# Kernel optimization log

Measured on AMD Instinct MI355X. Metric: run time of the kernel, lower is better.

## Reference

```python
import jax, jax.numpy as jnp
import numpy as np

EPS = 1e-5

def rotate_half(x):
    # interleaved pairs: (..., d*2) -> stack(-x2, x1) interleaved back
    x = x.reshape(*x.shape[:-1], -1, 2)
    x1, x2 = x[..., 0], x[..., 1]
    return jnp.stack((-x2, x1), axis=-1).reshape(*x.shape[:-2], -1)

def apply_rotary(freqs, x):
    # freqs: (b, n, d); x: (b, h, n, d) -> broadcast over heads (unsqueeze at dim=1)
    f = freqs[:, None, :, :]
    return x * jnp.cos(f) + rotate_half(x) * jnp.sin(f)

def layer_norm(x, g, b):
    mu = jnp.mean(x, axis=-1, keepdims=True)
    var = jnp.var(x, axis=-1, keepdims=True)
    return (x - mu) * jax.lax.rsqrt(var + EPS) * g + b

def setup_inputs() -> dict:
    key = jax.random.key(0)
    ks = jax.random.split(key, 10)
    b, nq, nkv, dim, h, dh = 8, 1024, 2048, 512, 8, 64
    inner = h * dh
    return {
        "x_query": jax.random.normal(ks[0], (b, nq, dim), jnp.float32),
        "x_context": jax.random.normal(ks[1], (b, nkv, dim), jnp.float32),
        "rotary_time_emb_query": jax.random.normal(ks[2], (b, nq, dh), jnp.float32),
        "rotary_time_emb_context": jax.random.normal(ks[3], (b, nkv, dh), jnp.float32),
        "context_mask": jnp.ones((b, nkv), dtype=bool),
        "ln_q_g": jnp.ones((dim,), jnp.float32),
        "ln_q_b": jnp.zeros((dim,), jnp.float32),
        "ln_c_g": jnp.ones((dim,), jnp.float32),
        "ln_c_b": jnp.zeros((dim,), jnp.float32),
        "Wq": jax.random.normal(ks[4], (dim, inner), jnp.float32) * 0.02,
        "Wkv": jax.random.normal(ks[5], (dim, 2 * inner), jnp.float32) * 0.02,
        "Wo": jax.random.normal(ks[6], (inner, dim), jnp.float32) * 0.02,
        "bo": jnp.zeros((dim,), jnp.float32),
    }

def reference(x_query, x_context, rotary_time_emb_query, rotary_time_emb_context,
              context_mask, ln_q_g, ln_q_b, ln_c_g, ln_c_b, Wq, Wkv, Wo, bo):
    h = 8
    xq = layer_norm(x_query, ln_q_g, ln_q_b)
    xc = layer_norm(x_context, ln_c_g, ln_c_b)
    q = xq @ Wq                       # (b, nq, inner)
    kv = xc @ Wkv                     # (b, nkv, 2*inner)
    k, v = jnp.split(kv, 2, axis=-1)
    split_heads = lambda t: t.reshape(t.shape[0], t.shape[1], h, -1).transpose(0, 2, 1, 3)
    q, k, v = split_heads(q), split_heads(k), split_heads(v)  # (b, h, n, dh)
    q = apply_rotary(rotary_time_emb_query, q)
    k = apply_rotary(rotary_time_emb_context, k)
    v = apply_rotary(rotary_time_emb_context, v)   # rotate_value=True
    dh = q.shape[-1]
    scale = 1.0 / jnp.sqrt(jnp.float32(dh))
    scores = jnp.einsum('bhqd,bhkd->bhqk', q, k) * scale
    neg = jnp.finfo(scores.dtype).min
    scores = jnp.where(context_mask[:, None, None, :], scores, neg)
    attn = jax.nn.softmax(scores, axis=-1)
    out = jnp.einsum('bhqk,bhkd->bhqd', attn, v)
    out = apply_rotary(-rotary_time_emb_query, out)  # inverse rotation
    out = out.transpose(0, 2, 1, 3).reshape(out.shape[0], out.shape[2], -1)  # (b, nq, inner)
    return out @ Wo + bo
```

## Files before the change

### kernel.cpp

```cpp
#include <hip/hip_runtime.h>
#include <hip/hip_bf16.h>
#include <math.h>

#define BB 8
#define NQ 1024
#define NKV 2048
#define DIM 512
#define H 8
#define DH 64
#define INNER 512
#define SCALE_LOG2E 0.18033688011112042f

typedef __bf16 bf16x8 __attribute__((ext_vector_type(8)));
typedef float f32x4 __attribute__((ext_vector_type(4)));
typedef unsigned int u32x4 __attribute__((ext_vector_type(4)));

__device__ __forceinline__ unsigned short f2bf(float f) {
  union { float f; unsigned int u; } v; v.f = f;
  unsigned int r = v.u + 0x7fffu + ((v.u >> 16) & 1u);
  return (unsigned short)(r >> 16);
}
__device__ __forceinline__ float bf2f(unsigned short h) {
  union { unsigned int u; float f; } v; v.u = ((unsigned int)h) << 16;
  return v.f;
}

__global__ __launch_bounds__(256) void prep_weights(
    const float* __restrict__ Wq, const float* __restrict__ Wkv,
    const float* __restrict__ Wo,
    unsigned short* __restrict__ WqT, unsigned short* __restrict__ WkvT,
    unsigned short* __restrict__ WohT, unsigned short* __restrict__ WolT) {
  __shared__ float T[64][65];
  int blk = blockIdx.x;
  const float* src; int Wd, ti, tj, mode;
  unsigned short* dst = nullptr;
  if (blk < 64) { src = Wq;  dst = WqT;  Wd = 512;  ti = blk >> 3; tj = blk & 7; mode = 0; }
  else if (blk < 192) { int b2 = blk - 64; src = Wkv; dst = WkvT; Wd = 1024; ti = b2 >> 4; tj = b2 & 15; mode = 0; }
  else { int b2 = blk - 192; src = Wo; Wd = 512; ti = b2 >> 3; tj = b2 & 7; mode = 1; }
  int t = threadIdx.x;
#pragma unroll
  for (int i = 0; i < 16; ++i) {
    int idx = i * 256 + t;
    int r = idx >> 6, c = idx & 63;
    T[r][c] = src[(size_t)(ti * 64 + r) * Wd + tj * 64 + c];
  }
  __syncthreads();
#pragma unroll
  for (int i = 0; i < 16; ++i) {
    int idx = i * 256 + t;
    int n = idx >> 6, k = idx & 63;
    float v = T[k][n];
    size_t off = (size_t)(tj * 64 + n) * 512 + ti * 64 + k;
    if (mode == 0) {
      dst[off] = f2bf(v);
    } else {
      unsigned short hb = f2bf(v);
      WohT[off] = hb;
      WolT[off] = f2bf(v - bf2f(hb));
    }
  }
}

__global__ __launch_bounds__(256) void ln_kernel(
    const float* __restrict__ xq, const float* __restrict__ xc,
    const float* __restrict__ gq, const float* __restrict__ bq,
    const float* __restrict__ gc, const float* __restrict__ bc,
    unsigned short* __restrict__ xq_bf, unsigned short* __restrict__ xc_bf) {
  int row = blockIdx.x;
  const float* x; const float* g; const float* bb; unsigned short* out;
  if (row < BB * NQ) {
    x = xq + (size_t)row * DIM; g = gq; bb = bq; out = xq_bf + (size_t)row * DIM;
  } else {
    int r = row - BB * NQ;
    x = xc + (size_t)r * DIM; g = gc; bb = bc; out = xc_bf + (size_t)r * DIM;
  }
  int t = threadIdx.x;
  float2 v = *reinterpret_cast<const float2*>(x + t * 2);
  float s = v.x + v.y;
  float ss = v.x * v.x + v.y * v.y;
#pragma unroll
  for (int d = 1; d < 64; d <<= 1) { s += __shfl_xor(s, d); ss += __shfl_xor(ss, d); }
  __shared__ float red[8];
  int wid = t >> 6, lane = t & 63;
  if (lane == 0) { red[wid] = s; red[4 + wid] = ss; }
  __syncthreads();
  s = red[0] + red[1] + red[2] + red[3];
  ss = red[4] + red[5] + red[6] + red[7];
  float mu = s * (1.0f / DIM);
  float var = ss * (1.0f / DIM) - mu * mu;
  float rs = rsqrtf(var + 1e-5f);
  float y0 = (v.x - mu) * rs * g[t * 2] + bb[t * 2];
  float y1 = (v.y - mu) * rs * g[t * 2 + 1] + bb[t * 2 + 1];
  ushort2 o; o.x = f2bf(y0); o.y = f2bf(y1);
  *reinterpret_cast<ushort2*>(out + t * 2) = o;
}

__device__ __forceinline__ void gemm_mainloop(
    const unsigned short* __restrict__ A, const unsigned short* __restrict__ WT,
    unsigned short* As, unsigned short* Ws, float (*Cs)[66],
    int rowBase, int colBase) {
  const int t = threadIdx.x;
  const int w = t >> 6;
  const int l = t & 63;
  const int l15 = l & 15;
  const int lg = l >> 4;
  const int c7 = l15 & 7;
  f32x4 acc[4];
#pragma unroll
  for (int ct = 0; ct < 4; ++ct) acc[ct] = f32x4{0.f, 0.f, 0.f, 0.f};
  const int arow = t >> 2;
  const int aseg = (t & 3) * 16;
  const int sdst0 = arow * 64 + ((2 * (t & 3)) ^ (arow & 7)) * 8;
  const int afrag = (lg ^ c7) * 8;
  const int ard = (w * 16 + l15) * 64 + afrag;
  const unsigned short* gab = A + (size_t)(rowBase + arow) * 512 + aseg;
  const unsigned short* gwb = WT + (size_t)(colBase + arow) * 512 + aseg;
  bf16x8 ar0 = *reinterpret_cast<const bf16x8*>(gab);
  bf16x8 ar1 = *reinterpret_cast<const bf16x8*>(gab + 8);
  bf16x8 wr0 = *reinterpret_cast<const bf16x8*>(gwb);
  bf16x8 wr1 = *reinterpret_cast<const bf16x8*>(gwb + 8);
  for (int kb = 0; kb < 512; kb += 64) {
    *reinterpret_cast<bf16x8*>(&As[sdst0])     = ar0;
    *reinterpret_cast<bf16x8*>(&As[sdst0 ^ 8]) = ar1;
    *reinterpret_cast<bf16x8*>(&Ws[sdst0])     = wr0;
    *reinterpret_cast<bf16x8*>(&Ws[sdst0 ^ 8]) = wr1;
    __syncthreads();
    if (kb + 64 < 512) {
      ar0 = *reinterpret_cast<const bf16x8*>(gab + kb + 64);
      ar1 = *reinterpret_cast<const bf16x8*>(gab + kb + 72);
      wr0 = *reinterpret_cast<const bf16x8*>(gwb + kb + 64);
      wr1 = *reinterpret_cast<const bf16x8*>(gwb + kb + 72);
    }
#pragma unroll
    for (int ks = 0; ks < 2; ++ks) {
      bf16x8 af = *reinterpret_cast<const bf16x8*>(&As[ard ^ (ks ? 32 : 0)]);
#pragma unroll
      for (int ct = 0; ct < 4; ++ct) {
        bf16x8 bfr = *reinterpret_cast<const bf16x8*>(
            &Ws[(ct * 16 + l15) * 64 + (afrag ^ (ks ? 32 : 0))]);
        acc[ct] = __builtin_amdgcn_mfma_f32_16x16x32_bf16(af, bfr, acc[ct], 0, 0, 0);
      }
    }
    __syncthreads();
  }
#pragma unroll
  for (int ct = 0; ct < 4; ++ct)
#pragma unroll
    for (int r = 0; r < 4; ++r)
      Cs[w * 16 + lg * 4 + r][ct * 16 + l15] = acc[ct][r];
  __syncthreads();
}

__global__ __launch_bounds__(256) void proj_q(
    const unsigned short* __restrict__ xq_bf, const unsigned short* __restrict__ WqT,
    const float* __restrict__ rotq, unsigned short* __restrict__ Qb) {
  __shared__ unsigned short As[64 * 64];
  __shared__ unsigned short Ws[64 * 64];
  __shared__ float Cs[64][66];
  int o = blockIdx.x;
  int swz = ((o & 7) << 7) + (o >> 3);
  int bn = swz & 7, bm = swz >> 3;
  gemm_mainloop(xq_bf, WqT, As, Ws, Cs, bm * 64, bn * 64);
  int t = threadIdx.x;
#pragma unroll
  for (int i = 0; i < 8; ++i) {
    int p = i * 256 + t;
    int row = p >> 5, pc = p & 31, d0 = pc * 2;
    int grow = bm * 64 + row;
    float c0 = Cs[row][d0], c1 = Cs[row][d0 + 1];
    const float* f = rotq + (size_t)grow * DH + d0;
    float f0 = f[0], f1 = f[1], s0, s1, co0, co1;
    __sincosf(f0, &s0, &co0);
    __sincosf(f1, &s1, &co1);
    float o0 = (c0 * co0 - c1 * s0) * SCALE_LOG2E;
    float o1 = (c1 * co1 + c0 * s1) * SCALE_LOG2E;
    ushort2 ov; ov.x = f2bf(o0); ov.y = f2bf(o1);
    int b = grow >> 10, qq = grow & 1023;
    *reinterpret_cast<ushort2*>(Qb + (((size_t)(b * H + bn) * NQ + qq) * DH + d0)) = ov;
  }
}

__global__ __launch_bounds__(256) void proj_kv(
    const unsigned short* __restrict__ xc_bf, const unsigned short* __restrict__ WkvT,
    const float* __restrict__ rotc, unsigned short* __restrict__ Kb,
    unsigned short* __restrict__ VTb) {
  __shared__ unsigned short As[64 * 64];
  __shared__ unsigned short Ws[64 * 64];
  __shared__ float Cs[64][66];
  int o = blockIdx.x;
  int swz = ((o & 7) << 9) + (o >> 3);
  int bn = swz & 15, bm = swz >> 4;
  gemm_mainloop(xc_bf, WkvT, As, Ws, Cs, bm * 64, bn * 64);
  int t = threadIdx.x;
  int h = bn & 7;
  int b = bm >> 5, chunk = bm & 31;
  if (bn < 8) {
#pragma unroll
    for (int i = 0; i < 8; ++i) {
      int p = i * 256 + t;
      int row = p >> 5, pc = p & 31, d0 = pc * 2;
      int grow = bm * 64 + row;
      float c0 = Cs[row][d0], c1 = Cs[row][d0 + 1];
      const float* f = rotc + (size_t)grow * DH + d0;
      float f0 = f[0], f1 = f[1], s0, s1, co0, co1;
      __sincosf(f0, &s0, &co0);
      __sincosf(f1, &s1, &co1);
      float o0 = c0 * co0 - c1 * s0;
      float o1 = c1 * co1 + c0 * s1;
      int kk = grow & 2047;
      ushort2 ov; ov.x = f2bf(o0); ov.y = f2bf(o1);
      *reinterpret_cast<ushort2*>(Kb + (((size_t)(b * H + h) * NKV + kk) * DH + d0)) = ov;
    }
  } else {
    unsigned short* vbase = VTb + (((size_t)(b * H + h) * 32 + chunk) * 64) * 64;
    int oc = t & 7;
    int dd0 = t >> 3;
#pragma unroll
    for (int half = 0; half < 2; ++half) {
      int d = dd0 + half * 32;
      u32x4 pack;
#pragma unroll
      for (int j2 = 0; j2 < 4; ++j2) {
        unsigned int lohi[2];
#pragma unroll
        for (int e = 0; e < 2; ++e) {
          int p = oc * 8 + j2 * 2 + e;
          int pp = p & 31;
          int kv = (p >> 5) * 32 + ((pp & 1) ? ((pp >> 1) + 16) : (pp >> 1));
          float c0 = Cs[kv][d], cx = Cs[kv][d ^ 1];
          float f = rotc[(size_t)(bm * 64 + kv) * DH + d];
          float sn, cs;
          __sincosf(f, &sn, &cs);
          float val = (d & 1) ? (c0 * cs + cx * sn) : (c0 * cs - cx * sn);
          lohi[e] = f2bf(val);
        }
        pack[j2] = lohi[0] | (lohi[1] << 16);
      }
      *reinterpret_cast<u32x4*>(vbase + d * 64 + oc * 8) = pack;
    }
  }
}

__global__ __launch_bounds__(256) void attn_kernel(
    const unsigned short* __restrict__ Qb, const unsigned short* __restrict__ Kb,
    const unsigned short* __restrict__ VTb, const int* __restrict__ mask,
    const float* __restrict__ rotq,
    unsigned short* __restrict__ Ahb, unsigned short* __restrict__ Alb) {
  __shared__ unsigned short Ks[64 * 64];
  __shared__ unsigned short Vs[64 * 64];
  __shared__ unsigned short Ps[4 * 16 * 64];
  __shared__ float Ms[NKV];
  int ob = blockIdx.x;
  int swz = ((ob & 7) << 7) + (ob >> 3);
  int qb = swz & 15;
  int bh = swz >> 4;
  int b = bh >> 3, hh = bh & 7;
  int t = threadIdx.x, w = t >> 6, l = t & 63;
  int l15 = l & 15, lg = l >> 4;
  int c7 = l15 & 7;

  {
    const int* mrow = mask + b * NKV;
    int4 m0 = *reinterpret_cast<const int4*>(mrow + t * 8);
    int4 m1 = *reinterpret_cast<const int4*>(mrow + t * 8 + 4);
    Ms[t * 8 + 0] = m0.x ? 1.f : 0.f;
    Ms[t * 8 + 1] = m0.y ? 1.f : 0.f;
    Ms[t * 8 + 2] = m0.z ? 1.f : 0.f;
    Ms[t * 8 + 3] = m0.w ? 1.f : 0.f;
    Ms[t * 8 + 4] = m1.x ? 1.f : 0.f;
    Ms[t * 8 + 5] = m1.y ? 1.f : 0.f;
    Ms[t * 8 + 6] = m1.z ? 1.f : 0.f;
    Ms[t * 8 + 7] = m1.w ? 1.f : 0.f;
  }

  const unsigned short* qrow = Qb + ((size_t)bh * NQ + qb * 64 + w * 16 + l15) * DH;
  bf16x8 qa0 = *reinterpret_cast<const bf16x8*>(qrow + lg * 8);
  bf16x8 qa1 = *reinterpret_cast<const bf16x8*>(qrow + 32 + lg * 8);

  float plsum[4] = {0.f, 0.f, 0.f, 0.f};
  f32x4 acc[4];
#pragma unroll
  for (int ct = 0; ct < 4; ++ct) acc[ct] = f32x4{0.f, 0.f, 0.f, 0.f};

  const int srow = t >> 2;
  const int sseg = (t & 3) * 16;
  const int sdst0 = srow * 64 + ((2 * (t & 3)) ^ (srow & 7)) * 8;
  const int frag = (lg ^ c7) * 8;
  const int kbase = l15 * 64 + frag;
  const int prbase = w * 1024 + l15 * 64 + frag;
  unsigned int* pw = reinterpret_cast<unsigned int*>(Ps);
  const int lg4 = lg * 4, l3 = l15 & 3, sD = l15 >> 2;

  const unsigned short* gk = Kb + ((size_t)bh * NKV + srow) * DH + sseg;
  const unsigned short* gv = VTb + (((size_t)bh * 32) * 64 + srow) * 64 + sseg;

  bf16x8 kr0 = *reinterpret_cast<const bf16x8*>(gk);
  bf16x8 kr1 = *reinterpret_cast<const bf16x8*>(gk + 8);
  bf16x8 vr0 = *reinterpret_cast<const bf16x8*>(gv);
  bf16x8 vr1 = *reinterpret_cast<const bf16x8*>(gv + 8);
  gk += 4096; gv += 4096;

  for (int ic = 0; ic < NKV / 64; ++ic) {
    *reinterpret_cast<bf16x8*>(&Ks[sdst0])     = kr0;
    *reinterpret_cast<bf16x8*>(&Ks[sdst0 ^ 8]) = kr1;
    *reinterpret_cast<bf16x8*>(&Vs[sdst0])     = vr0;
    *reinterpret_cast<bf16x8*>(&Vs[sdst0 ^ 8]) = vr1;
    __syncthreads();
    if (ic + 1 < NKV / 64) {
      kr0 = *reinterpret_cast<const bf16x8*>(gk);
      kr1 = *reinterpret_cast<const bf16x8*>(gk + 8);
      vr0 = *reinterpret_cast<const bf16x8*>(gv);
      vr1 = *reinterpret_cast<const bf16x8*>(gv + 8);
      gk += 4096; gv += 4096;
    }
    f32x4 s[4];
    __builtin_amdgcn_s_setprio(1);
#pragma unroll
    for (int tt = 0; tt < 4; ++tt) {
      f32x4 z = f32x4{0.f, 0.f, 0.f, 0.f};
      bf16x8 k0 = *reinterpret_cast<const bf16x8*>(&Ks[tt * 1024 + kbase]);
      z = __builtin_amdgcn_mfma_f32_16x16x32_bf16(qa0, k0, z, 0, 0, 0);
      bf16x8 k1 = *reinterpret_cast<const bf16x8*>(&Ks[tt * 1024 + (kbase ^ 32)]);
      z = __builtin_amdgcn_mfma_f32_16x16x32_bf16(qa1, k1, z, 0, 0, 0);
      s[tt] = z;
    }
    __builtin_amdgcn_s_setprio(0);
    float mv[4];
#pragma unroll
    for (int tt = 0; tt < 4; ++tt) mv[tt] = Ms[ic * 64 + tt * 16 + l15];
    float p[4][4];
#pragma unroll
    for (int tt = 0; tt < 4; ++tt)
#pragma unroll
      for (int r = 0; r < 4; ++r) {
        float e;
        asm("v_exp_f32 %0, %1" : "=v"(e) : "v"(s[tt][r]));
        p[tt][r] = e * mv[tt];
      }
#pragma unroll
    for (int r = 0; r < 4; ++r)
      plsum[r] += (p[0][r] + p[1][r]) + (p[2][r] + p[3][r]);
#pragma unroll
    for (int r = 0; r < 4; ++r) {
      unsigned int d01, d23;
      asm("v_cvt_pk_bf16_f32 %0, %1, %2" : "=v"(d01) : "v"(p[0][r]), "v"(p[1][r]));
      asm("v_cvt_pk_bf16_f32 %0, %1, %2" : "=v"(d23) : "v"(p[2][r]), "v"(p[3][r]));
      int row = lg4 + r;
      int rb = row & 7;
      int dwl = ((sD ^ rb) << 2) + l3;
      int pb = w * 512 + row * 32 + dwl;
      pw[pb] = d01;
      pw[pb ^ 16] = d23;
    }
    asm volatile("s_waitcnt lgkmcnt(0)" ::: "memory");
    __builtin_amdgcn_sched_barrier(0);
    __builtin_amdgcn_s_setprio(1);
#pragma unroll
    for (int ks = 0; ks < 2; ++ks) {
      bf16x8 pa = *reinterpret_cast<const bf16x8*>(&Ps[(prbase ^ (ks ? 32 : 0))]);
#pragma unroll
      for (int ct = 0; ct < 4; ++ct) {
        bf16x8 vb = *reinterpret_cast<const bf16x8*>(
            &Vs[ct * 1024 + (kbase ^ (ks ? 32 : 0))]);
        acc[ct] = __builtin_amdgcn_mfma_f32_16x16x32_bf16(pa, vb, acc[ct], 0, 0, 0);
      }
    }
    __builtin_amdgcn_s_setprio(0);
    __syncthreads();
  }
#pragma unroll
  for (int d = 1; d < 16; d <<= 1)
#pragma unroll
    for (int r = 0; r < 4; ++r) plsum[r] += __shfl_xor(plsum[r], d);
  float inv[4];
#pragma unroll
  for (int r = 0; r < 4; ++r) inv[r] = 1.0f / plsum[r];

  int q0 = qb * 64 + w * 16 + lg * 4;
#pragma unroll
  for (int r = 0; r < 4; ++r) {
    int grow = b * NQ + q0 + r;
    const float* frow = rotq + (size_t)grow * DH;
    size_t obase = (size_t)grow * INNER + hh * DH;
#pragma unroll
    for (int ct = 0; ct < 4; ++ct) {
      int d = ct * 16 + l15;
      float x = acc[ct][r] * inv[r];
      float nb = __shfl_xor(x, 1);
      float f = frow[d];
      float sn, cs;
      __sincosf(f, &sn, &cs);
      float ov = (d & 1) ? (x * cs - nb * sn) : (x * cs + nb * sn);
      unsigned short hb = f2bf(ov);
      Ahb[obase + d] = hb;
      Alb[obase + d] = f2bf(ov - bf2f(hb));
    }
  }
}

__global__ __launch_bounds__(256) void final_gemm(
    const unsigned short* __restrict__ Ah, const unsigned short* __restrict__ Al,
    const unsigned short* __restrict__ Wh, const unsigned short* __restrict__ Wl,
    const float* __restrict__ bo, float* __restrict__ out) {
  __shared__ unsigned short AhS[64 * 64];
  __shared__ unsigned short AlS[64 * 64];
  __shared__ unsigned short WhS[64 * 64];
  __shared__ unsigned short WlS[64 * 64];
  int o = blockIdx.x;
  int swz = ((o & 7) << 7) + (o >> 3);
  int bn = swz & 7, bm = swz >> 3;
  const int t = threadIdx.x;
  const int w = t >> 6, l = t & 63;
  const int l15 = l & 15, lg = l >> 4, c7 = l15 & 7;
  f32x4 acc[4];
#pragma unroll
  for (int ct = 0; ct < 4; ++ct) acc[ct] = f32x4{0.f, 0.f, 0.f, 0.f};
  const int arow = t >> 2;
  const int aseg = (t & 3) * 16;
  const int sdst0 = arow * 64 + ((2 * (t & 3)) ^ (arow & 7)) * 8;
  const int afrag = (lg ^ c7) * 8;
  const int ard = (w * 16 + l15) * 64 + afrag;
  const unsigned short* gah = Ah + (size_t)(bm * 64 + arow) * 512 + aseg;
  const unsigned short* gal = Al + (size_t)(bm * 64 + arow) * 512 + aseg;
  const unsigned short* gwh = Wh + (size_t)(bn * 64 + arow) * 512 + aseg;
  const unsigned short* gwl = Wl + (size_t)(bn * 64 + arow) * 512 + aseg;
  bf16x8 rah0 = *reinterpret_cast<const bf16x8*>(gah);
  bf16x8 rah1 = *reinterpret_cast<const bf16x8*>(gah + 8);
  bf16x8 ral0 = *reinterpret_cast<const bf16x8*>(gal);
  bf16x8 ral1 = *reinterpret_cast<const bf16x8*>(gal + 8);
  bf16x8 rwh0 = *reinterpret_cast<const bf16x8*>(gwh);
  bf16x8 rwh1 = *reinterpret_cast<const bf16x8*>(gwh + 8);
  bf16x8 rwl0 = *reinterpret_cast<const bf16x8*>(gwl);
  bf16x8 rwl1 = *reinterpret_cast<const bf16x8*>(gwl + 8);
  for (int kb = 0; kb < 512; kb += 64) {
    *reinterpret_cast<bf16x8*>(&AhS[sdst0])     = rah0;
    *reinterpret_cast<bf16x8*>(&AhS[sdst0 ^ 8]) = rah1;
    *reinterpret_cast<bf16x8*>(&AlS[sdst0])     = ral0;
    *reinterpret_cast<bf16x8*>(&AlS[sdst0 ^ 8]) = ral1;
    *reinterpret_cast<bf16x8*>(&WhS[sdst0])     = rwh0;
    *reinterpret_cast<bf16x8*>(&WhS[sdst0 ^ 8]) = rwh1;
    *reinterpret_cast<bf16x8*>(&WlS[sdst0])     = rwl0;
    *reinterpret_cast<bf16x8*>(&WlS[sdst0 ^ 8]) = rwl1;
    __syncthreads();
    if (kb + 64 < 512) {
      rah0 = *reinterpret_cast<const bf16x8*>(gah + kb + 64);
      rah1 = *reinterpret_cast<const bf16x8*>(gah + kb + 72);
      ral0 = *reinterpret_cast<const bf16x8*>(gal + kb + 64);
      ral1 = *reinterpret_cast<const bf16x8*>(gal + kb + 72);
      rwh0 = *reinterpret_cast<const bf16x8*>(gwh + kb + 64);
      rwh1 = *reinterpret_cast<const bf16x8*>(gwh + kb + 72);
      rwl0 = *reinterpret_cast<const bf16x8*>(gwl + kb + 64);
      rwl1 = *reinterpret_cast<const bf16x8*>(gwl + kb + 72);
    }
#pragma unroll
    for (int ks = 0; ks < 2; ++ks) {
      const int x = ks ? 32 : 0;
      bf16x8 ah = *reinterpret_cast<const bf16x8*>(&AhS[ard ^ x]);
      bf16x8 al = *reinterpret_cast<const bf16x8*>(&AlS[ard ^ x]);
#pragma unroll
      for (int ct = 0; ct < 4; ++ct) {
        const int wb = (ct * 16 + l15) * 64 + (afrag ^ x);
        bf16x8 wh = *reinterpret_cast<const bf16x8*>(&WhS[wb]);
        bf16x8 wl = *reinterpret_cast<const bf16x8*>(&WlS[wb]);
        acc[ct] = __builtin_amdgcn_mfma_f32_16x16x32_bf16(ah, wh, acc[ct], 0, 0, 0);
        acc[ct] = __builtin_amdgcn_mfma_f32_16x16x32_bf16(al, wh, acc[ct], 0, 0, 0);
        acc[ct] = __builtin_amdgcn_mfma_f32_16x16x32_bf16(ah, wl, acc[ct], 0, 0, 0);
      }
    }
    __syncthreads();
  }
  int row0 = bm * 64 + w * 16 + lg * 4;
#pragma unroll
  for (int ct = 0; ct < 4; ++ct) {
    int col = bn * 64 + ct * 16 + l15;
    float bv = bo[col];
#pragma unroll
    for (int r = 0; r < 4; ++r)
      out[(size_t)(row0 + r) * 512 + col] = acc[ct][r] + bv;
  }
}

extern "C" void kernel_launch(void* const* d_in, const int* in_sizes, int n_in,
                              void* d_out, int out_size, void* d_ws, size_t ws_size,
                              hipStream_t stream) {
  const float* x_query   = (const float*)d_in[0];
  const float* x_context = (const float*)d_in[1];
  const float* rot_q     = (const float*)d_in[2];
  const float* rot_c     = (const float*)d_in[3];
  const int*   cmask     = (const int*)d_in[4];
  const float* ln_q_g    = (const float*)d_in[5];
  const float* ln_q_b    = (const float*)d_in[6];
  const float* ln_c_g    = (const float*)d_in[7];
  const float* ln_c_b    = (const float*)d_in[8];
  const float* Wq        = (const float*)d_in[9];
  const float* Wkv       = (const float*)d_in[10];
  const float* Wo        = (const float*)d_in[11];
  const float* bo        = (const float*)d_in[12];
  float* out = (float*)d_out;

  char* ws = (char*)d_ws;
  unsigned short* xq_bf = (unsigned short*)(ws + 0);
  unsigned short* xc_bf = (unsigned short*)(ws + 8388608);
  unsigned short* Ahb   = (unsigned short*)(ws + 0);
  unsigned short* Alb   = (unsigned short*)(ws + 8388608);
  unsigned short* WqT   = (unsigned short*)(ws + 25165824);
  unsigned short* WkvT  = (unsigned short*)(ws + 25690112);
  unsigned short* Qb    = (unsigned short*)(ws + 26738688);
  unsigned short* Kb    = (unsigned short*)(ws + 35127296);
  unsigned short* VTb   = (unsigned short*)(ws + 51904512);
  unsigned short* WohT  = (unsigned short*)(ws + 68681728);
  unsigned short* WolT  = (unsigned short*)(ws + 69206016);

  prep_weights<<<dim3(256), dim3(256), 0, stream>>>(Wq, Wkv, Wo, WqT, WkvT, WohT, WolT);
  ln_kernel<<<dim3(24576), dim3(256), 0, stream>>>(x_query, x_context, ln_q_g, ln_q_b,
                                                   ln_c_g, ln_c_b, xq_bf, xc_bf);
  proj_q<<<dim3(1024), dim3(256), 0, stream>>>(xq_bf, WqT, rot_q, Qb);
  proj_kv<<<dim3(4096), dim3(256), 0, stream>>>(xc_bf, WkvT, rot_c, Kb, VTb);
  attn_kernel<<<dim3(1024), dim3(256), 0, stream>>>(Qb, Kb, VTb, cmask, rot_q, Ahb, Alb);
  final_gemm<<<dim3(1024), dim3(256), 0, stream>>>(Ahb, Alb, WohT, WolT, bo, out);
}
```

Measured before the change: 155.4 us.

## Fold key mask into K/V projection and double-buffer attention K/V tiles

```diff
diff --git a/kernel.cpp b/kernel.cpp
--- a/kernel.cpp
+++ b/kernel.cpp
@@ -182,8 +182,8 @@
 
 __global__ __launch_bounds__(256) void proj_kv(
     const unsigned short* __restrict__ xc_bf, const unsigned short* __restrict__ WkvT,
-    const float* __restrict__ rotc, unsigned short* __restrict__ Kb,
-    unsigned short* __restrict__ VTb) {
+    const float* __restrict__ rotc, const int* __restrict__ cmask,
+    unsigned short* __restrict__ Kb, unsigned short* __restrict__ VTb) {
   __shared__ unsigned short As[64 * 64];
   __shared__ unsigned short Ws[64 * 64];
   __shared__ float Cs[64][66];
@@ -205,8 +205,9 @@
       float f0 = f[0], f1 = f[1], s0, s1, co0, co1;
       __sincosf(f0, &s0, &co0);
       __sincosf(f1, &s1, &co1);
-      float o0 = c0 * co0 - c1 * s0;
-      float o1 = c1 * co1 + c0 * s1;
+      float mf = cmask[grow] ? 1.f : 0.f;
+      float o0 = (c0 * co0 - c1 * s0) * mf;
+      float o1 = (c1 * co1 + c0 * s1) * mf;
       int kk = grow & 2047;
       ushort2 ov; ov.x = f2bf(o0); ov.y = f2bf(o1);
       *reinterpret_cast<ushort2*>(Kb + (((size_t)(b * H + h) * NKV + kk) * DH + d0)) = ov;
@@ -231,7 +232,8 @@
           float f = rotc[(size_t)(bm * 64 + kv) * DH + d];
           float sn, cs;
           __sincosf(f, &sn, &cs);
-          float val = (d & 1) ? (c0 * cs + cx * sn) : (c0 * cs - cx * sn);
+          float mf = cmask[bm * 64 + kv] ? 1.f : 0.f;
+          float val = ((d & 1) ? (c0 * cs + cx * sn) : (c0 * cs - cx * sn)) * mf;
           lohi[e] = f2bf(val);
         }
         pack[j2] = lohi[0] | (lohi[1] << 16);
@@ -246,10 +248,9 @@
     const unsigned short* __restrict__ VTb, const int* __restrict__ mask,
     const float* __restrict__ rotq,
     unsigned short* __restrict__ Ahb, unsigned short* __restrict__ Alb) {
-  __shared__ unsigned short Ks[64 * 64];
-  __shared__ unsigned short Vs[64 * 64];
+  __shared__ unsigned short Ks[2 * 64 * 64];
+  __shared__ unsigned short Vs[2 * 64 * 64];
   __shared__ unsigned short Ps[4 * 16 * 64];
-  __shared__ float Ms[NKV];
   int ob = blockIdx.x;
   int swz = ((ob & 7) << 7) + (ob >> 3);
   int qb = swz & 15;
@@ -259,18 +260,19 @@
   int l15 = l & 15, lg = l >> 4;
   int c7 = l15 & 7;
 
+  float nmasked;
   {
     const int* mrow = mask + b * NKV;
-    int4 m0 = *reinterpret_cast<const int4*>(mrow + t * 8);
-    int4 m1 = *reinterpret_cast<const int4*>(mrow + t * 8 + 4);
-    Ms[t * 8 + 0] = m0.x ? 1.f : 0.f;
-    Ms[t * 8 + 1] = m0.y ? 1.f : 0.f;
-    Ms[t * 8 + 2] = m0.z ? 1.f : 0.f;
-    Ms[t * 8 + 3] = m0.w ? 1.f : 0.f;
-    Ms[t * 8 + 4] = m1.x ? 1.f : 0.f;
-    Ms[t * 8 + 5] = m1.y ? 1.f : 0.f;
-    Ms[t * 8 + 6] = m1.z ? 1.f : 0.f;
-    Ms[t * 8 + 7] = m1.w ? 1.f : 0.f;
+    float msum = 0.f;
+#pragma unroll
+    for (int i = 0; i < 8; ++i) {
+      int4 m = *reinterpret_cast<const int4*>(mrow + l * 4 + i * 256);
+      msum += (m.x ? 1.f : 0.f) + (m.y ? 1.f : 0.f) +
+              (m.z ? 1.f : 0.f) + (m.w ? 1.f : 0.f);
+    }
+#pragma unroll
+    for (int d = 1; d < 64; d <<= 1) msum += __shfl_xor(msum, d);
+    nmasked = (float)NKV - msum;
   }
 
   const unsigned short* qrow = Qb + ((size_t)bh * NQ + qb * 64 + w * 16 + l15) * DH;
@@ -300,11 +302,13 @@
   bf16x8 vr1 = *reinterpret_cast<const bf16x8*>(gv + 8);
   gk += 4096; gv += 4096;
 
+#pragma unroll 2
   for (int ic = 0; ic < NKV / 64; ++ic) {
-    *reinterpret_cast<bf16x8*>(&Ks[sdst0])     = kr0;
-    *reinterpret_cast<bf16x8*>(&Ks[sdst0 ^ 8]) = kr1;
-    *reinterpret_cast<bf16x8*>(&Vs[sdst0])     = vr0;
-    *reinterpret_cast<bf16x8*>(&Vs[sdst0 ^ 8]) = vr1;
+    const int bo_ = (ic & 1) << 12;
+    *reinterpret_cast<bf16x8*>(&Ks[bo_ + sdst0])       = kr0;
+    *reinterpret_cast<bf16x8*>(&Ks[bo_ + (sdst0 ^ 8)]) = kr1;
+    *reinterpret_cast<bf16x8*>(&Vs[bo_ + sdst0])       = vr0;
+    *reinterpret_cast<bf16x8*>(&Vs[bo_ + (sdst0 ^ 8)]) = vr1;
     __syncthreads();
     if (ic + 1 < NKV / 64) {
       kr0 = *reinterpret_cast<const bf16x8*>(gk);
@@ -318,16 +322,13 @@
 #pragma unroll
     for (int tt = 0; tt < 4; ++tt) {
       f32x4 z = f32x4{0.f, 0.f, 0.f, 0.f};
-      bf16x8 k0 = *reinterpret_cast<const bf16x8*>(&Ks[tt * 1024 + kbase]);
+      bf16x8 k0 = *reinterpret_cast<const bf16x8*>(&Ks[bo_ + tt * 1024 + kbase]);
       z = __builtin_amdgcn_mfma_f32_16x16x32_bf16(qa0, k0, z, 0, 0, 0);
-      bf16x8 k1 = *reinterpret_cast<const bf16x8*>(&Ks[tt * 1024 + (kbase ^ 32)]);
+      bf16x8 k1 = *reinterpret_cast<const bf16x8*>(&Ks[bo_ + tt * 1024 + (kbase ^ 32)]);
       z = __builtin_amdgcn_mfma_f32_16x16x32_bf16(qa1, k1, z, 0, 0, 0);
       s[tt] = z;
     }
     __builtin_amdgcn_s_setprio(0);
-    float mv[4];
-#pragma unroll
-    for (int tt = 0; tt < 4; ++tt) mv[tt] = Ms[ic * 64 + tt * 16 + l15];
     float p[4][4];
 #pragma unroll
     for (int tt = 0; tt < 4; ++tt)
@@ -335,7 +336,7 @@
       for (int r = 0; r < 4; ++r) {
         float e;
         asm("v_exp_f32 %0, %1" : "=v"(e) : "v"(s[tt][r]));
-        p[tt][r] = e * mv[tt];
+        p[tt][r] = e;
       }
 #pragma unroll
     for (int r = 0; r < 4; ++r)
@@ -361,12 +362,11 @@
 #pragma unroll
       for (int ct = 0; ct < 4; ++ct) {
         bf16x8 vb = *reinterpret_cast<const bf16x8*>(
-            &Vs[ct * 1024 + (kbase ^ (ks ? 32 : 0))]);
+            &Vs[bo_ + ct * 1024 + (kbase ^ (ks ? 32 : 0))]);
         acc[ct] = __builtin_amdgcn_mfma_f32_16x16x32_bf16(pa, vb, acc[ct], 0, 0, 0);
       }
     }
     __builtin_amdgcn_s_setprio(0);
-    __syncthreads();
   }
 #pragma unroll
   for (int d = 1; d < 16; d <<= 1)
@@ -374,7 +374,7 @@
     for (int r = 0; r < 4; ++r) plsum[r] += __shfl_xor(plsum[r], d);
   float inv[4];
 #pragma unroll
-  for (int r = 0; r < 4; ++r) inv[r] = 1.0f / plsum[r];
+  for (int r = 0; r < 4; ++r) inv[r] = 1.0f / (plsum[r] - nmasked);
 
   int q0 = qb * 64 + w * 16 + lg * 4;
 #pragma unroll
@@ -515,7 +515,7 @@
   ln_kernel<<<dim3(24576), dim3(256), 0, stream>>>(x_query, x_context, ln_q_g, ln_q_b,
                                                    ln_c_g, ln_c_b, xq_bf, xc_bf);
   proj_q<<<dim3(1024), dim3(256), 0, stream>>>(xq_bf, WqT, rot_q, Qb);
-  proj_kv<<<dim3(4096), dim3(256), 0, stream>>>(xc_bf, WkvT, rot_c, Kb, VTb);
+  proj_kv<<<dim3(4096), dim3(256), 0, stream>>>(xc_bf, WkvT, rot_c, cmask, Kb, VTb);
   attn_kernel<<<dim3(1024), dim3(256), 0, stream>>>(Qb, Kb, VTb, cmask, rot_q, Ahb, Alb);
   final_gemm<<<dim3(1024), dim3(256), 0, stream>>>(Ahb, Alb, WohT, WolT, bo, out);
 }
```

Measured after the change: 154.7 us. Within noise of the previous version (-0.4%).
